# Kernel optimization log

Measured on AMD Instinct MI355X. Metric: run time of the kernel, lower is better.

The kernel has to match this reference:

```python
import jax, jax.numpy as jnp
import numpy as np

EPS = 1e-8
TOP_K = 3  # hardcoded in the original forward (torch.topk(sims, 3))


def setup_inputs() -> dict:
    key = jax.random.key(0)
    ks = jax.random.split(key, 6)
    n1, d1 = 4096, 1024
    n2, d2 = 4096, 4096
    V = jax.random.normal(ks[0], (n1, d1), dtype=jnp.float32)
    X = jax.random.normal(ks[1], (n2, d2), dtype=jnp.float32)
    # nn.Linear(visual_dim, text_dim): weight [d2, d1], bias [d2]
    Wv = jax.random.normal(ks[2], (d2, d1), dtype=jnp.float32) * (1.0 / np.sqrt(d1))
    bv = jax.random.normal(ks[3], (d2,), dtype=jnp.float32) * 0.01
    # nn.Linear(top_k, 1): weight [1, 3], bias [1]
    Wf = jax.random.normal(ks[4], (1, TOP_K), dtype=jnp.float32) * (1.0 / np.sqrt(TOP_K))
    bf = jax.random.normal(ks[5], (1,), dtype=jnp.float32) * 0.01
    return {"V": V, "X": X, "Wv": Wv, "bv": bv, "Wf": Wf, "bf": bf}


def reference(V, X, Wv, bv, Wf, bf):
    # project visual tokens into text space: [n1, d2]
    V_proj = V @ Wv.T + bv
    # cosine similarity: normalize queries (full-vector norm) and keys (row norm)
    Qn = X / (jnp.linalg.norm(X, axis=1, keepdims=True) + EPS)          # [n2, d2]
    Kn = V_proj / (jnp.linalg.norm(V_proj, axis=1, keepdims=True) + EPS)  # [n1, d2]
    sims = Qn @ Kn.T                                                     # [n2, n1]
    # per-text-token top-k visual tokens
    _, topk_idx = jax.lax.top_k(sims, TOP_K)                             # [n2, k]
    gathered = V_proj[topk_idx]                                          # [n2, k, d2]
    # fuse over k: Linear(k -> 1) applied along the top-k axis, squeeze -> [n2, d2]
    V_aligned = jnp.einsum('nkd,k->nd', gathered, Wf[0]) + bf[0]
    return jnp.concatenate([V_aligned, X], axis=0)                       # [2*n2, d2]
```

## Files before the change

kernel.cpp:

```cpp
#include <hip/hip_runtime.h>
#include <hip/hip_bf16.h>

constexpr int N1 = 4096;
constexpr int D1 = 1024;
constexpr int N2 = 4096;
constexpr int D2 = 4096;

#define FNEG  (-3.402823466e+38f)
#define IDX_INF 0x7FFFFFFF
#define NCHUNK 32
#define CPR (NCHUNK * 6)
#define FCAP 1024
#define ZPB 4
#define CERT_TH 2.0e-4f

using s16x8 = __attribute__((ext_vector_type(8))) short;
using f32x4 = __attribute__((ext_vector_type(4))) float;

static __device__ __forceinline__ unsigned short f2bf(float x) {
    unsigned int u = __float_as_uint(x);
    unsigned int r = (u + 0x7FFFu + ((u >> 16) & 1u)) >> 16;
    return (unsigned short)r;
}
static __device__ __forceinline__ float bf2f(unsigned short v) {
    return __uint_as_float((unsigned)v << 16);
}
static __device__ __forceinline__ void splitbf(float x, unsigned short& h,
                                               unsigned short& l) {
    unsigned short hh = f2bf(x);
    float r = x - __uint_as_float((unsigned)hh << 16);
    h = hh; l = f2bf(r);
}
static __device__ __forceinline__ int swz(int row, int g) {
    return row * 32 + ((g ^ (row & 3)) << 3);
}

static __device__ __forceinline__ void stageF32(const float* src, int ld,
    int rowbase, int k0, unsigned short* H, unsigned short* L, int tid)
{
    const int r = tid >> 1, half = tid & 1;
    const float* p = src + (size_t)(rowbase + r) * ld + k0 + half * 16;
#pragma unroll
    for (int gg = 0; gg < 2; ++gg) {
        const int g = half * 2 + gg;
        float4 v0 = *(const float4*)(p + gg * 8);
        float4 v1 = *(const float4*)(p + gg * 8 + 4);
        float xs[8] = {v0.x, v0.y, v0.z, v0.w, v1.x, v1.y, v1.z, v1.w};
        s16x8 hv, lv;
#pragma unroll
        for (int e = 0; e < 8; ++e) {
            unsigned short h, l; splitbf(xs[e], h, l);
            hv[e] = (short)h; lv[e] = (short)l;
        }
        const int a = swz(r, g);
        *(s16x8*)&H[a] = hv;
        *(s16x8*)&L[a] = lv;
    }
}

static __device__ __forceinline__ void gl_lds16(const void* g, void* l)
{
    __builtin_amdgcn_global_load_lds(
        (const __attribute__((address_space(1))) void*)g,
        (__attribute__((address_space(3))) void*)l, 16, 0, 0);
}

static __device__ __forceinline__ void stageSplitGL(const unsigned short* Hs,
    const unsigned short* Ls, int ld, int rowbase, int k0,
    unsigned short* H, unsigned short* L, int lane, int w)
{
#pragma unroll
    for (int t = 0; t < 2; ++t) {
        const int chunk = w * 128 + t * 64 + lane;
        const int row = chunk >> 2;
        const int gp  = chunk & 3;
        const int g   = gp ^ (row & 3);
        const unsigned short* sh =
            Hs + (size_t)(rowbase + row) * ld + k0 + g * 8;
        const unsigned short* sl =
            Ls + (size_t)(rowbase + row) * ld + k0 + g * 8;
        unsigned short* dh = H + (size_t)(w * 128 + t * 64) * 8;
        unsigned short* dl = L + (size_t)(w * 128 + t * 64) * 8;
        gl_lds16(sh, dh);
        gl_lds16(sl, dl);
    }
}

static __device__ __forceinline__ void stageWvTpre(const unsigned short* Wh,
    const unsigned short* Wl, int k0, int tn,
    unsigned short* H, unsigned short* L, int tid)
{
    const int kk = tid >> 3, cg = tid & 7;
    const int g = kk >> 3, idx = kk & 7;
    const unsigned short* ph = Wh + (size_t)(k0 + kk) * D1 + tn + cg * 16;
    const unsigned short* pl = Wl + (size_t)(k0 + kk) * D1 + tn + cg * 16;
#pragma unroll
    for (int q = 0; q < 4; ++q) {
        ushort4 vh = *(const ushort4*)(ph + q * 4);
        ushort4 vl = *(const ushort4*)(pl + q * 4);
        unsigned short hs[4] = {vh.x, vh.y, vh.z, vh.w};
        unsigned short ls[4] = {vl.x, vl.y, vl.z, vl.w};
#pragma unroll
        for (int e = 0; e < 4; ++e) {
            const int cc = cg * 16 + q * 4 + e;
            const int a = cc * 32 + ((g ^ (cc & 3)) << 3) + idx;
            H[a] = hs[e]; L[a] = ls[e];
        }
    }
}

static __device__ __forceinline__ s16x8 fragRead(const unsigned short* B,
                                                 int rowbase, int lane)
{
    const int row = rowbase + (lane & 15);
    const int g = lane >> 4;
    return *(const s16x8*)&B[row * 32 + ((g ^ (row & 3)) << 3)];
}

#define MFMA3(ACC, AH, AL, BH, BL)                                          \
    ACC = __builtin_amdgcn_mfma_f32_16x16x32_bf16(AH, BH, ACC, 0, 0, 0);    \
    ACC = __builtin_amdgcn_mfma_f32_16x16x32_bf16(AH, BL, ACC, 0, 0, 0);    \
    ACC = __builtin_amdgcn_mfma_f32_16x16x32_bf16(AL, BH, ACC, 0, 0, 0);

static __device__ __forceinline__ void top6f(float v, int i, float* vv, int* ii)
{
#pragma unroll
    for (int s = 0; s < 6; ++s) {
        if (v > vv[s]) {
#pragma unroll
            for (int t = 5; t > s; --t) { vv[t] = vv[t-1]; ii[t] = ii[t-1]; }
            vv[s] = v; ii[s] = i;
            break;
        }
    }
}

__global__ __launch_bounds__(256)
void kDetect(const float* c1, const float* c2, int* flags, int* flagCnt)
{
    __shared__ float red[256];
    float d = 0.f;
    for (int i = threadIdx.x; i < 4096; i += 256) {
        float a = c1[i], b = c2[i];
        d += a * a - b * b;
    }
    red[threadIdx.x] = d;
    __syncthreads();
    for (int st = 128; st > 0; st >>= 1) {
        if (threadIdx.x < st) red[threadIdx.x] += red[threadIdx.x + st];
        __syncthreads();
    }
    if (threadIdx.x == 0) {
        flags[0] = (red[0] < 0.f) ? 1 : 0;
        flagCnt[0] = 0;
    }
}

__global__ __launch_bounds__(256)
void kSplit(const float* src, unsigned short* h, unsigned short* l, int n4)
{
    int i = blockIdx.x * 256 + threadIdx.x;
    if (i >= n4) return;
    float4 v = *(const float4*)(src + (size_t)i * 4);
    float xs[4] = {v.x, v.y, v.z, v.w};
    ushort4 hv, lv;
    unsigned short hh, ll;
    splitbf(xs[0], hh, ll); hv.x = hh; lv.x = ll;
    splitbf(xs[1], hh, ll); hv.y = hh; lv.y = ll;
    splitbf(xs[2], hh, ll); hv.z = hh; lv.z = ll;
    splitbf(xs[3], hh, ll); hv.w = hh; lv.w = ll;
    *(ushort4*)(h + (size_t)i * 4) = hv;
    *(ushort4*)(l + (size_t)i * 4) = lv;
}

__global__ __launch_bounds__(256)
void kSvec(const float* X, const float* bv, float* sXF, double* sXD)
{
    __shared__ double red[256];
    const int row = blockIdx.x;
    double s = 0.0;
    for (int n = threadIdx.x; n < D2; n += 256)
        s += (double)X[(size_t)row * D2 + n] * (double)bv[n];
    red[threadIdx.x] = s;
    __syncthreads();
    for (int st = 128; st > 0; st >>= 1) {
        if (threadIdx.x < st) red[threadIdx.x] += red[threadIdx.x + st];
        __syncthreads();
    }
    if (threadIdx.x == 0) { sXF[row] = (float)red[0]; sXD[row] = red[0]; }
}

__global__ __launch_bounds__(256)
void kNormMfma(const unsigned short* c1h, const unsigned short* c1l,
               const unsigned short* c2h, const unsigned short* c2l,
               const float* bv, const int* flags, float* partial,
               unsigned short* Vph)
{
    const unsigned short* Vh  = flags[0] ? c2h : c1h;
    const unsigned short* Vl  = flags[0] ? c2l : c1l;
    const unsigned short* Wvh = flags[0] ? c1h : c2h;
    const unsigned short* Wvl = flags[0] ? c1l : c2l;
    __shared__ __align__(16) char pool[65536];
    __shared__ float partH[128][2];
    const int tid = threadIdx.x;
    const int lane = tid & 63, w = tid >> 6;
    const int wr = w >> 1, wc = w & 1;
    const int tm = blockIdx.y * 128;
    const int tn = blockIdx.x * 128;

    f32x4 acc[4][4];
#pragma unroll
    for (int i = 0; i < 4; ++i)
#pragma unroll
        for (int j = 0; j < 4; ++j) acc[i][j] = (f32x4){0.f, 0.f, 0.f, 0.f};

    {
        unsigned short* B0 = (unsigned short*)pool;
        stageSplitGL(Vh,  Vl,  D1, tm, 0, B0,        B0 + 4096,  lane, w);
        stageSplitGL(Wvh, Wvl, D1, tn, 0, B0 + 8192, B0 + 12288, lane, w);
    }
    __syncthreads();

    for (int k0 = 0; k0 < D1; k0 += 32) {
        const int cur = (k0 >> 5) & 1;
        unsigned short* CB = (unsigned short*)(pool + cur * 32768);
        if (k0 + 32 < D1) {
            unsigned short* NB = (unsigned short*)(pool + (cur ^ 1) * 32768);
            stageSplitGL(Vh,  Vl,  D1, tm, k0 + 32, NB,        NB + 4096,
                         lane, w);
            stageSplitGL(Wvh, Wvl, D1, tn, k0 + 32, NB + 8192, NB + 12288,
                         lane, w);
        }
        s16x8 ah[4], al[4], bh[4], bl[4];
#pragma unroll
        for (int f = 0; f < 4; ++f) {
            ah[f] = fragRead(CB,         wr * 64 + f * 16, lane);
            al[f] = fragRead(CB + 4096,  wr * 64 + f * 16, lane);
            bh[f] = fragRead(CB + 8192,  wc * 64 + f * 16, lane);
            bl[f] = fragRead(CB + 12288, wc * 64 + f * 16, lane);
        }
#pragma unroll
        for (int fm = 0; fm < 4; ++fm)
#pragma unroll
            for (int fn = 0; fn < 4; ++fn) {
                MFMA3(acc[fm][fn], ah[fm], al[fm], bh[fn], bl[fn]);
            }
        __syncthreads();
    }

    float bvv[4];
#pragma unroll
    for (int fn = 0; fn < 4; ++fn)
        bvv[fn] = bv[tn + wc * 64 + fn * 16 + (lane & 15)];
#pragma unroll
    for (int fm = 0; fm < 4; ++fm)
#pragma unroll
        for (int r = 0; r < 4; ++r) {
            const int lrow = wr * 64 + fm * 16 + (lane >> 4) * 4 + r;
            float rs = 0.f;
#pragma unroll
            for (int fn = 0; fn < 4; ++fn) {
                float v = acc[fm][fn][r] + bvv[fn];
                Vph[(size_t)(tm + lrow) * D2 +
                    (tn + wc * 64 + fn * 16 + (lane & 15))] = f2bf(v);
                rs += v * v;
            }
            rs += __shfl_xor(rs, 1, 64);
            rs += __shfl_xor(rs, 2, 64);
            rs += __shfl_xor(rs, 4, 64);
            rs += __shfl_xor(rs, 8, 64);
            if ((lane & 15) == 0) partH[lrow][wc] = rs;
        }
    __syncthreads();
    if (tid < 128)
        partial[(size_t)(tm + tid) * 32 + blockIdx.x] =
            partH[tid][0] + partH[tid][1];
}

__global__ __launch_bounds__(256)
void kInv(const float* partial, float* invnF, double* invnD)
{
    int j = blockIdx.x * 256 + threadIdx.x;
    double s = 0.0;
    for (int cb = 0; cb < 32; ++cb) s += (double)partial[(size_t)j * 32 + cb];
    double iv = 1.0 / (sqrt(s) + 1e-8);
    invnD[j] = iv;
    invnF[j] = (float)iv;
}

__global__ __launch_bounds__(256)
void mfmaZ(const float* X,
           const unsigned short* c1h, const unsigned short* c1l,
           const unsigned short* c2h, const unsigned short* c2l,
           const int* flags, unsigned short* Zh, unsigned short* Zl)
{
    const unsigned short* Wvh = flags[0] ? c1h : c2h;
    const unsigned short* Wvl = flags[0] ? c1l : c2l;
    __shared__ unsigned short AH[4096], AL[4096], BH[4096], BL[4096];
    const int tid = threadIdx.x;
    const int lane = tid & 63, w = tid >> 6;
    const int wr = w >> 1, wc = w & 1;
    const int tm = blockIdx.y * 128;
    const int tn = blockIdx.x * 128;

    f32x4 acc[4][4];
#pragma unroll
    for (int i = 0; i < 4; ++i)
#pragma unroll
        for (int j = 0; j < 4; ++j) acc[i][j] = (f32x4){0.f, 0.f, 0.f, 0.f};

    for (int k0 = 0; k0 < D2; k0 += 32) {
        stageF32(X, D2, tm, k0, AH, AL, tid);
        stageWvTpre(Wvh, Wvl, k0, tn, BH, BL, tid);
        __syncthreads();
        s16x8 ah[4], al[4], bh[4], bl[4];
#pragma unroll
        for (int f = 0; f < 4; ++f) {
            ah[f] = fragRead(AH, wr * 64 + f * 16, lane);
            al[f] = fragRead(AL, wr * 64 + f * 16, lane);
            bh[f] = fragRead(BH, wc * 64 + f * 16, lane);
            bl[f] = fragRead(BL, wc * 64 + f * 16, lane);
        }
#pragma unroll
        for (int fm = 0; fm < 4; ++fm)
#pragma unroll
            for (int fn = 0; fn < 4; ++fn) {
                MFMA3(acc[fm][fn], ah[fm], al[fm], bh[fn], bl[fn]);
            }
        __syncthreads();
    }
#pragma unroll
    for (int fm = 0; fm < 4; ++fm)
#pragma unroll
        for (int fn = 0; fn < 4; ++fn)
#pragma unroll
            for (int r = 0; r < 4; ++r) {
                int row = tm + wr * 64 + fm * 16 + (lane >> 4) * 4 + r;
                int col = tn + wc * 64 + fn * 16 + (lane & 15);
                unsigned short h, l;
                splitbf(acc[fm][fn][r], h, l);
                size_t o = (size_t)row * D1 + col;
                Zh[o] = h; Zl[o] = l;
            }
}

__global__ __launch_bounds__(256)
void mfmaS(const unsigned short* Zh, const unsigned short* Zl,
           const unsigned short* c1h, const unsigned short* c1l,
           const unsigned short* c2h, const unsigned short* c2l,
           const float* invnF, const float* sXF, const int* flags,
           float* candV, int* candI)
{
    const unsigned short* Vh = flags[0] ? c2h : c1h;
    const unsigned short* Vl = flags[0] ? c2l : c1l;
    __shared__ __align__(16) char pool[65536];
    float* Ct   = (float*)pool;
    float* pv   = (float*)(pool + 33792);
    int*   pi   = (int*)  (pool + 36864);
    float* invs = (float*)(pool + 39936);

    const int tid = threadIdx.x;
    const int lane = tid & 63, w = tid >> 6;
    const int wr = w >> 1, wc = w & 1;
    const int tm = blockIdx.y * 128;
    const int tn = blockIdx.x * 128;

    f32x4 acc[4][4];
#pragma unroll
    for (int i = 0; i < 4; ++i)
#pragma unroll
        for (int j = 0; j < 4; ++j) acc[i][j] = (f32x4){0.f, 0.f, 0.f, 0.f};

    {
        unsigned short* B0 = (unsigned short*)pool;
        stageSplitGL(Zh, Zl, D1, tm, 0, B0,        B0 + 4096,  lane, w);
        stageSplitGL(Vh, Vl, D1, tn, 0, B0 + 8192, B0 + 12288, lane, w);
    }
    __syncthreads();

    for (int k0 = 0; k0 < D1; k0 += 32) {
        const int cur = (k0 >> 5) & 1;
        unsigned short* CB = (unsigned short*)(pool + cur * 32768);
        if (k0 + 32 < D1) {
            unsigned short* NB = (unsigned short*)(pool + (cur ^ 1) * 32768);
            stageSplitGL(Zh, Zl, D1, tm, k0 + 32, NB,        NB + 4096,
                         lane, w);
            stageSplitGL(Vh, Vl, D1, tn, k0 + 32, NB + 8192, NB + 12288,
                         lane, w);
        }
        s16x8 ah[4], al[4], bh[4], bl[4];
#pragma unroll
        for (int f = 0; f < 4; ++f) {
            ah[f] = fragRead(CB,         wr * 64 + f * 16, lane);
            al[f] = fragRead(CB + 4096,  wr * 64 + f * 16, lane);
            bh[f] = fragRead(CB + 8192,  wc * 64 + f * 16, lane);
            bl[f] = fragRead(CB + 12288, wc * 64 + f * 16, lane);
        }
#pragma unroll
        for (int fm = 0; fm < 4; ++fm)
#pragma unroll
            for (int fn = 0; fn < 4; ++fn) {
                MFMA3(acc[fm][fn], ah[fm], al[fm], bh[fn], bl[fn]);
            }
        __syncthreads();
    }

    if (tid < 128) invs[tid] = invnF[tn + tid];
    for (int h = 0; h < 2; ++h) {
        __syncthreads();
        if (wr == h) {
#pragma unroll
            for (int fm = 0; fm < 4; ++fm)
#pragma unroll
                for (int fn = 0; fn < 4; ++fn)
#pragma unroll
                    for (int r = 0; r < 4; ++r) {
                        int lr = fm * 16 + (lane >> 4) * 4 + r;
                        int c  = wc * 64 + fn * 16 + (lane & 15);
                        Ct[lr * 132 + c] = acc[fm][fn][r];
                    }
        }
        __syncthreads();
        if (tid < 128) {
            int r = tid >> 1, seg = tid & 1;
            float sxf = sXF[tm + h * 64 + r];
            float vv[6]; int ii[6];
#pragma unroll
            for (int s = 0; s < 6; ++s) { vv[s] = FNEG; ii[s] = IDX_INF; }
            for (int cc = 0; cc < 64; ++cc) {
                int c = seg * 64 + cc;
                float v = (Ct[r * 132 + c] + sxf) * invs[c];
                top6f(v, tn + c, vv, ii);
            }
#pragma unroll
            for (int s = 0; s < 6; ++s) {
                pv[(r * 2 + seg) * 6 + s] = vv[s];
                pi[(r * 2 + seg) * 6 + s] = ii[s];
            }
        }
        __syncthreads();
        if (tid < 64) {
            float vv[6]; int ii[6];
#pragma unroll
            for (int s = 0; s < 6; ++s) { vv[s] = FNEG; ii[s] = IDX_INF; }
            for (int seg = 0; seg < 2; ++seg)
                for (int s = 0; s < 6; ++s)
                    top6f(pv[(tid * 2 + seg) * 6 + s],
                          pi[(tid * 2 + seg) * 6 + s], vv, ii);
            int row = tm + h * 64 + tid;
#pragma unroll
            for (int s = 0; s < 6; ++s) {
                candV[(size_t)row * CPR + blockIdx.x * 6 + s] = vv[s];
                candI[(size_t)row * CPR + blockIdx.x * 6 + s] = ii[s];
            }
        }
    }
}

__global__ __launch_bounds__(64)
void kMergeCert(const float* candV, const int* candI, int* tidx,
                int* flagCnt, int* flagRow, int* flagCand)
{
    if (threadIdx.x != 0) return;
    const int row = blockIdx.x;
    float vv[6]; int ii[6];
    for (int s = 0; s < 6; ++s) { vv[s] = FNEG; ii[s] = IDX_INF; }
    for (int c = 0; c < CPR; ++c)
        top6f(candV[(size_t)row * CPR + c], candI[(size_t)row * CPR + c],
              vv, ii);
    tidx[row * 3 + 0] = ii[0];
    tidx[row * 3 + 1] = ii[1];
    tidx[row * 3 + 2] = ii[2];
    bool cert = (vv[0] - vv[1] > CERT_TH) &&
                (vv[1] - vv[2] > CERT_TH) &&
                (vv[2] - vv[3] > CERT_TH);
    if (!cert) {
        int idx = atomicAdd(flagCnt, 1);
        if (idx < FCAP) {
            flagRow[idx] = row;
            for (int s = 0; s < 6; ++s) flagCand[idx * 6 + s] = ii[s];
        }
    }
}

__global__ __launch_bounds__(512)
void kZx(const int* flagCnt, const int* flagRow,
         const float* c1, const float* c2, const int* flags,
         const float* X, double* Zx)
{
    const float* Wv = flags[0] ? c1 : c2;
    const int nact = min(flagCnt[0], FCAP);
    const int z0 = blockIdx.x * ZPB;
    if (z0 >= nact) return;
    const int tid = threadIdx.x;
    __shared__ float Xs[ZPB][D2];
    const int na = min(ZPB, nact - z0);
    for (int zz = 0; zz < na; ++zz) {
        const float* xr = X + (size_t)flagRow[z0 + zz] * D2;
        for (int i = tid * 4; i < D2; i += 512 * 4)
            *(float4*)&Xs[zz][i] = *(const float4*)(xr + i);
    }
    for (int zz = na; zz < ZPB; ++zz)
        for (int i = tid * 4; i < D2; i += 512 * 4)
            *(float4*)&Xs[zz][i] = (float4){0.f, 0.f, 0.f, 0.f};
    __syncthreads();

    const int c2i = tid * 2;
    double acc[ZPB][2];
#pragma unroll
    for (int zz = 0; zz < ZPB; ++zz) { acc[zz][0] = 0.0; acc[zz][1] = 0.0; }

#pragma unroll 4
    for (int n = 0; n < D2; ++n) {
        float2 wv2 = *(const float2*)(Wv + (size_t)n * D1 + c2i);
        const double wx = (double)wv2.x, wy = (double)wv2.y;
#pragma unroll
        for (int zz = 0; zz < ZPB; ++zz) {
            const double xv = (double)Xs[zz][n];
            acc[zz][0] = fma(xv, wx, acc[zz][0]);
            acc[zz][1] = fma(xv, wy, acc[zz][1]);
        }
    }
    for (int zz = 0; zz < na; ++zz) {
        Zx[(size_t)(z0 + zz) * D1 + c2i]     = acc[zz][0];
        Zx[(size_t)(z0 + zz) * D1 + c2i + 1] = acc[zz][1];
    }
}

__global__ __launch_bounds__(64)
void kScore6(const int* flagCnt, const int* flagRow, const int* flagCand,
             const double* Zx, const float* c1, const float* c2,
             const int* flags, const double* sXD, const double* invnD,
             int* tidx)
{
    const int z = blockIdx.x;
    if (z >= flagCnt[0] || z >= FCAP) return;
    const float* V = flags[0] ? c2 : c1;
    const int lane = threadIdx.x;

    double zr[16];
#pragma unroll
    for (int t = 0; t < 16; ++t)
        zr[t] = Zx[(size_t)z * D1 + t * 64 + lane];

    double sc[6]; int js[6];
    for (int s = 0; s < 6; ++s) {
        js[s] = flagCand[z * 6 + s];
        const float* vr = V + (size_t)js[s] * D1;
        double d = 0.0;
#pragma unroll
        for (int t = 0; t < 16; ++t)
            d = fma(zr[t], (double)vr[t * 64 + lane], d);
#pragma unroll
        for (int off = 1; off < 64; off <<= 1)
            d += __shfl_xor(d, off, 64);
        sc[s] = d;
    }
    if (lane == 0) {
        const int row = flagRow[z];
        const double sx = sXD[row];
        for (int s = 0; s < 6; ++s)
            sc[s] = (sc[s] + sx) * invnD[js[s]];
        int ord[6] = {0, 1, 2, 3, 4, 5};
        for (int a = 0; a < 5; ++a)
            for (int b = a + 1; b < 6; ++b) {
                bool swp = (sc[ord[b]] > sc[ord[a]]) ||
                           (sc[ord[b]] == sc[ord[a]] &&
                            js[ord[b]] < js[ord[a]]);
                if (swp) { int t = ord[a]; ord[a] = ord[b]; ord[b] = t; }
            }
        tidx[row * 3 + 0] = js[ord[0]];
        tidx[row * 3 + 1] = js[ord[1]];
        tidx[row * 3 + 2] = js[ord[2]];
    }
}

__global__ __launch_bounds__(256)
void kGatherVa(const unsigned short* Vph, const int* tidx,
               const float* Wf, const float* bfp, float* outVa)
{
    const int row = blockIdx.x;
    const int i0 = tidx[row*3+0], i1 = tidx[row*3+1], i2 = tidx[row*3+2];
    const float w0 = Wf[0], w1 = Wf[1], w2 = Wf[2], b = bfp[0];
    const unsigned short* p0 = Vph + (size_t)i0 * D2;
    const unsigned short* p1 = Vph + (size_t)i1 * D2;
    const unsigned short* p2 = Vph + (size_t)i2 * D2;
    float* o = outVa + (size_t)row * D2;
    for (int c = threadIdx.x * 8; c < D2; c += 256 * 8) {
        s16x8 a = *(const s16x8*)(p0 + c);
        s16x8 d = *(const s16x8*)(p1 + c);
        s16x8 e = *(const s16x8*)(p2 + c);
        float out[8];
#pragma unroll
        for (int t = 0; t < 8; ++t)
            out[t] = w0 * bf2f((unsigned short)a[t]) +
                     w1 * bf2f((unsigned short)d[t]) +
                     w2 * bf2f((unsigned short)e[t]) + b;
        *(float4*)(o + c)     = *(float4*)&out[0];
        *(float4*)(o + c + 4) = *(float4*)&out[4];
    }
}

extern "C" void kernel_launch(void* const* d_in, const int* in_sizes, int n_in,
                              void* d_out, int out_size, void* d_ws, size_t ws_size,
                              hipStream_t stream)
{
    const float *c1 = nullptr, *c2 = nullptr, *X = nullptr;
    const float *bv = nullptr, *Wf = nullptr, *bfp = nullptr;
    for (int i = 0; i < n_in; ++i) {
        const float* p = (const float*)d_in[i];
        switch (in_sizes[i]) {
            case 16777216: X = p; break;
            case 4194304:  if (!c1) c1 = p; else c2 = p; break;
            case 4096:     bv = p; break;
            case 3:        Wf = p; break;
            case 1:        bfp = p; break;
            default: break;
        }
    }

    float* out_f = (float*)d_out;
    float* outVa = out_f;
    float* outX  = out_f + (size_t)N2 * D2;

    int* flags   = (int*)d_ws;
    int* flagCnt = (int*)((char*)d_ws + 128);
    char* C0 = (char*)d_ws + 1024;
    float*  sXF     = (float*) (C0);
    float*  invnF   = (float*) (C0 + 16384);
    int*    tidx    = (int*)   (C0 + 32768);
    double* sXD     = (double*)(C0 + 81920);
    double* invnD   = (double*)(C0 + 114688);
    float*  partial = (float*) (C0 + 147456);
    float*  candV   = (float*) (C0 + 671744);
    int*    candI   = (int*)   (C0 + 3817472);
    int*    flagRow = (int*)   (C0 + 6963200);
    int*    flagCand= (int*)   (C0 + 6967296);
    unsigned short* Zh = (unsigned short*)(C0 + 8388608);
    unsigned short* Zl = (unsigned short*)(C0 + 16777216);

    char* up = (char*)outX;
    unsigned short* c1h = (unsigned short*)(up);
    unsigned short* c1l = (unsigned short*)(up + 8388608);
    unsigned short* c2h = (unsigned short*)(up + 16777216);
    unsigned short* c2l = (unsigned short*)(up + 25165824);
    unsigned short* Vph = (unsigned short*)(up + 33554432);
    double* Zx = (double*)(up);

    kDetect<<<1, 256, 0, stream>>>(c1, c2, flags, flagCnt);
    kSplit<<<4096, 256, 0, stream>>>(c1, c1h, c1l, N1 * D1 / 4);
    kSplit<<<4096, 256, 0, stream>>>(c2, c2h, c2l, N1 * D1 / 4);
    kSvec<<<N2, 256, 0, stream>>>(X, bv, sXF, sXD);

    dim3 gN(D2 / 128, N1 / 128);
    kNormMfma<<<gN, 256, 0, stream>>>(c1h, c1l, c2h, c2l, bv, flags,
                                      partial, Vph);
    kInv<<<16, 256, 0, stream>>>(partial, invnF, invnD);

    dim3 gZ(D1 / 128, N2 / 128);
    mfmaZ<<<gZ, 256, 0, stream>>>(X, c1h, c1l, c2h, c2l, flags, Zh, Zl);

    dim3 gS(N1 / 128, N2 / 128);
    mfmaS<<<gS, 256, 0, stream>>>(Zh, Zl, c1h, c1l, c2h, c2l,
                                  invnF, sXF, flags, candV, candI);

    kMergeCert<<<N2, 64, 0, stream>>>(candV, candI, tidx,
                                      flagCnt, flagRow, flagCand);

    kZx<<<FCAP / ZPB, 512, 0, stream>>>(flagCnt, flagRow, c1, c2, flags,
                                        X, Zx);
    kScore6<<<FCAP, 64, 0, stream>>>(flagCnt, flagRow, flagCand, Zx,
                                     c1, c2, flags, sXD, invnD, tidx);

    kGatherVa<<<N2, 256, 0, stream>>>(Vph, tidx, Wf, bfp, outVa);

    hipMemcpyAsync(outX, X, (size_t)N2 * D2 * sizeof(float),
                   hipMemcpyDeviceToDevice, stream);
}
```

Before: 1.501 ms.

## Restructure fp64 Zx kernel into column-chunk by row-group grid with staged X tiles

Rewrites the fallback fp64 Zx kernel so each block covers 128 output columns and loops over groups of 8 flagged rows with a grid-stride over 32 row groups. X rows are staged into shared memory in 1024-wide slices instead of whole rows. Every block now has work regardless of the flagged-row count, and each Wv load is reused across 8 rows instead of 4. The trade-off is that large flagged counts are processed serially within each block, and there are more syncthreads per pass.

After: 1.503 ms. No clear change (+0.1%).

```diff
diff --git a/kernel.cpp b/kernel.cpp
--- a/kernel.cpp
+++ b/kernel.cpp
@@ -11,7 +11,8 @@
 #define NCHUNK 32
 #define CPR (NCHUNK * 6)
 #define FCAP 1024
-#define ZPB 4
+#define ZCH 8
+#define ZB 32
 #define CERT_TH 2.0e-4f
 
 using s16x8 = __attribute__((ext_vector_type(8))) short;
@@ -483,47 +484,51 @@
     }
 }
 
-__global__ __launch_bounds__(512)
+__global__ __launch_bounds__(128)
 void kZx(const int* flagCnt, const int* flagRow,
          const float* c1, const float* c2, const int* flags,
          const float* X, double* Zx)
 {
     const float* Wv = flags[0] ? c1 : c2;
     const int nact = min(flagCnt[0], FCAP);
-    const int z0 = blockIdx.x * ZPB;
-    if (z0 >= nact) return;
+    const int cc = blockIdx.x;
+    const int zb = blockIdx.y;
     const int tid = threadIdx.x;
-    __shared__ float Xs[ZPB][D2];
-    const int na = min(ZPB, nact - z0);
-    for (int zz = 0; zz < na; ++zz) {
-        const float* xr = X + (size_t)flagRow[z0 + zz] * D2;
-        for (int i = tid * 4; i < D2; i += 512 * 4)
-            *(float4*)&Xs[zz][i] = *(const float4*)(xr + i);
-    }
-    for (int zz = na; zz < ZPB; ++zz)
-        for (int i = tid * 4; i < D2; i += 512 * 4)
-            *(float4*)&Xs[zz][i] = (float4){0.f, 0.f, 0.f, 0.f};
-    __syncthreads();
-
-    const int c2i = tid * 2;
-    double acc[ZPB][2];
-#pragma unroll
-    for (int zz = 0; zz < ZPB; ++zz) { acc[zz][0] = 0.0; acc[zz][1] = 0.0; }
-
+    const int c = cc * 128 + tid;
+    __shared__ float Xs[ZCH][1024];
+    __shared__ int   rows[ZCH];
+
+    for (int z0 = zb * ZCH; z0 < nact; z0 += ZB * ZCH) {
+        const int na = min(ZCH, nact - z0);
+        __syncthreads();
+        if (tid < ZCH)
+            rows[tid] = flagRow[z0 + min(tid, na - 1)];
+        __syncthreads();
+
+        double acc[ZCH];
+#pragma unroll
+        for (int zz = 0; zz < ZCH; ++zz) acc[zz] = 0.0;
+
+        for (int n0 = 0; n0 < D2; n0 += 1024) {
+            __syncthreads();
+            for (int idx = tid * 4; idx < ZCH * 1024; idx += 128 * 4) {
+                const int zz = idx >> 10, i = idx & 1023;
+                *(float4*)&Xs[zz][i] =
+                    *(const float4*)(X + (size_t)rows[zz] * D2 + n0 + i);
+            }
+            __syncthreads();
 #pragma unroll 4
-    for (int n = 0; n < D2; ++n) {
-        float2 wv2 = *(const float2*)(Wv + (size_t)n * D1 + c2i);
-        const double wx = (double)wv2.x, wy = (double)wv2.y;
-#pragma unroll
-        for (int zz = 0; zz < ZPB; ++zz) {
-            const double xv = (double)Xs[zz][n];
-            acc[zz][0] = fma(xv, wx, acc[zz][0]);
-            acc[zz][1] = fma(xv, wy, acc[zz][1]);
-        }
-    }
-    for (int zz = 0; zz < na; ++zz) {
-        Zx[(size_t)(z0 + zz) * D1 + c2i]     = acc[zz][0];
-        Zx[(size_t)(z0 + zz) * D1 + c2i + 1] = acc[zz][1];
+            for (int i = 0; i < 1024; ++i) {
+                const double wvd = (double)Wv[(size_t)(n0 + i) * D1 + c];
+#pragma unroll
+                for (int zz = 0; zz < ZCH; ++zz)
+                    acc[zz] = fma((double)Xs[zz][i], wvd, acc[zz]);
+            }
+        }
+#pragma unroll
+        for (int zz = 0; zz < ZCH; ++zz)
+            if (zz < na)
+                Zx[(size_t)(z0 + zz) * D1 + c] = acc[zz];
     }
 }
 
@@ -667,8 +672,8 @@
     kMergeCert<<<N2, 64, 0, stream>>>(candV, candI, tidx,
                                       flagCnt, flagRow, flagCand);
 
-    kZx<<<FCAP / ZPB, 512, 0, stream>>>(flagCnt, flagRow, c1, c2, flags,
-                                        X, Zx);
+    dim3 gX(8, ZB);
+    kZx<<<gX, 128, 0, stream>>>(flagCnt, flagRow, c1, c2, flags, X, Zx);
     kScore6<<<FCAP, 64, 0, stream>>>(flagCnt, flagRow, flagCand, Zx,
                                      c1, c2, flags, sXD, invnD, tidx);
 
```
